# Kernel optimization log

Measured on AMD Instinct MI355X. Metric: run time of the kernel, lower is better.

The kernel has to match this reference:

```python
import jax, jax.numpy as jnp
import numpy as np

B, T, D = 4, 2048, 1024
H = 16
HD = D // H  # 64

def setup_inputs() -> dict:
    key = jax.random.key(0)
    k1, k2, k3, k4, k5 = jax.random.split(key, 5)
    s = 1.0 / np.sqrt(D)
    return {
        "x": jax.random.normal(k1, (B, T, D), dtype=jnp.float32),
        "Wqkv": jax.random.normal(k2, (D, 3 * D), dtype=jnp.float32) * s,
        "bqkv": jnp.zeros((3 * D,), dtype=jnp.float32),
        "Wproj": jax.random.normal(k3, (D, D), dtype=jnp.float32) * s,
        "bproj": jnp.zeros((D,), dtype=jnp.float32),
    }

def reference(x, Wqkv, bqkv, Wproj, bproj):
    Bq, Tq, C = x.shape
    qkv = x @ Wqkv + bqkv                       # [B,T,3D]
    qkv = qkv.reshape(Bq, Tq, 3, H, HD).transpose(2, 0, 3, 1, 4)  # [3,B,H,T,hd]
    q, k, v = qkv[0], qkv[1], qkv[2]
    scale = 1.0 / np.sqrt(HD)
    att = jnp.einsum("bhqd,bhkd->bhqk", q, k) * scale  # [B,H,T,T]
    causal = jnp.tril(jnp.ones((Tq, Tq), dtype=bool))
    att = jnp.where(causal[None, None], att, -jnp.inf)
    att = jax.nn.softmax(att, axis=-1)
    out = jnp.einsum("bhqk,bhkd->bhqd", att, v)        # [B,H,T,hd]
    out = out.transpose(0, 2, 1, 3).reshape(Bq, Tq, C)
    return out @ Wproj + bproj
```

## Files before the change

### kernel.cpp

```cpp
#include <hip/hip_runtime.h>

typedef float f32x4 __attribute__((ext_vector_type(4)));
typedef __bf16 bf16x8 __attribute__((ext_vector_type(8)));
typedef __bf16 bf16x4 __attribute__((ext_vector_type(4)));

#define B_ 4
#define T_ 2048
#define D_ 1024
#define H_ 16
#define HD_ 64

__device__ __forceinline__ void gload_lds16(const void* g, void* l) {
  __builtin_amdgcn_global_load_lds(
      (const __attribute__((address_space(1))) void*)g,
      (__attribute__((address_space(3))) void*)l, 16, 0, 0);
}

__global__ __launch_bounds__(256) void k_cvt_f32_bf16(
    const float* __restrict__ in, __bf16* __restrict__ out, int n4) {
  int i = blockIdx.x * blockDim.x + threadIdx.x;
  int stride = gridDim.x * blockDim.x;
  for (; i < n4; i += stride) {
    float4 v = reinterpret_cast<const float4*>(in)[i];
    bf16x4 o = { (__bf16)v.x, (__bf16)v.y, (__bf16)v.z, (__bf16)v.w };
    reinterpret_cast<bf16x4*>(out)[i] = o;
  }
}

template <typename Tin>
__global__ __launch_bounds__(256) void k_transpose_bf16(
    const Tin* __restrict__ in, __bf16* __restrict__ out,
    int R, int C, long inb, long outb) {
  __shared__ alignas(16) __bf16 lds[64 * 68];
  const int t = threadIdx.x;
  in  += (long)blockIdx.z * inb;
  out += (long)blockIdx.z * outb;
  const int r0 = blockIdx.y * 64, c0 = blockIdx.x * 64;
#pragma unroll
  for (int i = 0; i < 16; ++i) {
    int e = i * 256 + t, row = e >> 6, col = e & 63;
    lds[row * 68 + col] = (__bf16)(float)in[(long)(r0 + row) * C + c0 + col];
  }
  __syncthreads();
#pragma unroll
  for (int i = 0; i < 16; ++i) {
    int e = i * 256 + t, orow = e >> 6, ocol = e & 63;
    out[(long)(c0 + orow) * R + r0 + ocol] = lds[ocol * 68 + orow];
  }
}

template <int EPI>
__global__ __launch_bounds__(256) void k_gemm_bt(
    const __bf16* __restrict__ A, const __bf16* __restrict__ Bt,
    const float* __restrict__ bias, void* __restrict__ Cout,
    __bf16* __restrict__ vout, int M, int N, int K) {
  __shared__ alignas(16) __bf16 As[2][128 * 32];
  __shared__ alignas(16) __bf16 Bs[2][128 * 32];
  const int t = threadIdx.x;
  const int w = t >> 6, l = t & 63;
  const int g = l >> 4, r16 = l & 15;
  const int wr = w >> 1, wc = w & 1;
  const int m0 = blockIdx.y * 128, n0 = blockIdx.x * 128;

  f32x4 acc[4][4];
#pragma unroll
  for (int i = 0; i < 4; ++i)
#pragma unroll
    for (int j = 0; j < 4; ++j) acc[i][j] = (f32x4){0.f, 0.f, 0.f, 0.f};

  const int arow = t >> 2;
  const int acol = ((t & 3) ^ ((t >> 3) & 3)) * 8;
  const char* Ag = (const char*)(A + (long)(m0 + arow) * K + acol);
  const char* Bg = (const char*)(Bt + (long)(n0 + arow) * K + acol);
  const long rowskip = (long)64 * K * 2;
  const int rdsw = (g ^ ((r16 >> 1) & 3)) * 8;

  auto stage = [&](int buf, long koff) {
    char* AsW = (char*)As[buf] + w * 1024;
    char* BsW = (char*)Bs[buf] + w * 1024;
    gload_lds16(Ag + koff, AsW);
    gload_lds16(Ag + koff + rowskip, AsW + 4096);
    gload_lds16(Bg + koff, BsW);
    gload_lds16(Bg + koff + rowskip, BsW + 4096);
  };

  stage(0, 0);
  __syncthreads();

  for (int kt = 0; kt < K; kt += 32) {
    const int cur = (kt >> 5) & 1;
    if (kt + 32 < K) stage(cur ^ 1, (long)(kt + 32) * 2);
    bf16x8 af[4], bfr[4];
#pragma unroll
    for (int mi = 0; mi < 4; ++mi)
      af[mi] = *reinterpret_cast<const bf16x8*>(
          &As[cur][(wr * 64 + mi * 16 + r16) * 32 + rdsw]);
#pragma unroll
    for (int ni = 0; ni < 4; ++ni)
      bfr[ni] = *reinterpret_cast<const bf16x8*>(
          &Bs[cur][(wc * 64 + ni * 16 + r16) * 32 + rdsw]);
    __builtin_amdgcn_s_setprio(1);
#pragma unroll
    for (int mi = 0; mi < 4; ++mi)
#pragma unroll
      for (int ni = 0; ni < 4; ++ni)
        acc[mi][ni] = __builtin_amdgcn_mfma_f32_16x16x32_bf16(af[mi], bfr[ni], acc[mi][ni], 0, 0, 0);
    __builtin_amdgcn_s_setprio(0);
    __syncthreads();
  }

  if (EPI == 0) {
    const int which = n0 >> 10;
    __bf16* qkvb = (__bf16*)Cout;
#pragma unroll
    for (int mi = 0; mi < 4; ++mi) {
#pragma unroll
      for (int ni = 0; ni < 4; ++ni) {
        const int n = n0 + wc * 64 + ni * 16 + r16;
        const float bv = bias[n];
        f32x4 c = acc[mi][ni];
        const int rem = n & 1023, h = rem >> 6, hd = rem & 63;
        const int mbase = m0 + wr * 64 + mi * 16 + g * 4;
        const int b = mbase >> 11, tt0 = mbase & 2047;
        if (which < 2) {
#pragma unroll
          for (int r = 0; r < 4; ++r)
            qkvb[((long)((which * B_ + b) * H_ + h) * T_ + tt0 + r) * HD_ + hd] =
                (__bf16)(c[r] + bv);
        } else {
          bf16x4 pk = { (__bf16)(c[0] + bv), (__bf16)(c[1] + bv),
                        (__bf16)(c[2] + bv), (__bf16)(c[3] + bv) };
          *reinterpret_cast<bf16x4*>(
              &vout[(((long)b * H_ + h) * HD_ + hd) * T_ + tt0]) = pk;
        }
      }
    }
  } else {
    float* O = (float*)Cout;
#pragma unroll
    for (int mi = 0; mi < 4; ++mi) {
#pragma unroll
      for (int ni = 0; ni < 4; ++ni) {
        const int n = n0 + wc * 64 + ni * 16 + r16;
        const float bv = bias[n];
        f32x4 c = acc[mi][ni];
        const int mbase = m0 + wr * 64 + mi * 16 + g * 4;
#pragma unroll
        for (int r = 0; r < 4; ++r) O[(long)(mbase + r) * N + n] = c[r] + bv;
      }
    }
  }
}

__device__ __forceinline__ void soft_side(
    const f32x4 (&s)[4], float& lrun, bool diag, int qrel,
    int g, int r16, bf16x8& pa0, bf16x8& pa1) {
  float p[4][4];
#pragma unroll
  for (int nf = 0; nf < 4; ++nf) {
#pragma unroll
    for (int rr = 0; rr < 4; ++rr) {
      float x = s[nf][rr];
      if (diag) x = (nf * 16 + 4 * g + rr <= qrel + r16) ? x : -1e30f;
      p[nf][rr] = __builtin_amdgcn_exp2f(x);
    }
  }
  const float ps0 = (p[0][0] + p[0][1]) + (p[0][2] + p[0][3]);
  const float ps1 = (p[1][0] + p[1][1]) + (p[1][2] + p[1][3]);
  const float ps2 = (p[2][0] + p[2][1]) + (p[2][2] + p[2][3]);
  const float ps3 = (p[3][0] + p[3][1]) + (p[3][2] + p[3][3]);
  lrun += (ps0 + ps1) + (ps2 + ps3);

  unsigned u[4][2];
#pragma unroll
  for (int nf = 0; nf < 4; ++nf) {
    asm("v_cvt_pk_bf16_f32 %0, %1, %2"
        : "=v"(u[nf][0]) : "v"(p[nf][0]), "v"(p[nf][1]));
    asm("v_cvt_pk_bf16_f32 %0, %1, %2"
        : "=v"(u[nf][1]) : "v"(p[nf][2]), "v"(p[nf][3]));
  }
#pragma unroll
  for (int j = 0; j < 2; ++j) {
    asm("v_permlane32_swap_b32 %0, %1" : "+v"(u[0][j]), "+v"(u[1][j]));
    asm("v_permlane32_swap_b32 %0, %1" : "+v"(u[2][j]), "+v"(u[3][j]));
  }
#pragma unroll
  for (int j = 0; j < 2; ++j) {
    asm("v_permlane16_swap_b32 %0, %1" : "+v"(u[0][j]), "+v"(u[1][j]));
    asm("v_permlane16_swap_b32 %0, %1" : "+v"(u[2][j]), "+v"(u[3][j]));
  }
  union PU { unsigned w[4]; bf16x8 v; };
  PU a0, a1;
  a0.w[0] = u[0][0]; a0.w[1] = u[0][1]; a0.w[2] = u[1][0]; a0.w[3] = u[1][1];
  a1.w[0] = u[2][0]; a1.w[1] = u[2][1]; a1.w[2] = u[3][0]; a1.w[3] = u[3][1];
  pa0 = a0.v;
  pa1 = a1.v;
}

__global__ __launch_bounds__(256) void k_attn(
    const __bf16* __restrict__ q, const __bf16* __restrict__ k,
    const __bf16* __restrict__ vt, __bf16* __restrict__ o) {
  __shared__ alignas(16) __bf16 Ks[2][64 * 64];
  __shared__ alignas(16) __bf16 Vs[2][64 * 64];
  const int t = threadIdx.x, w = t >> 6, l = t & 63;
  const int g = l >> 4, r16 = l & 15;
  const int bh = blockIdx.x;
  const int prmap[16] = {0, 2, 4, 6, 15, 13, 11, 9, 1, 3, 5, 7, 14, 12, 10, 8};
  const int pr = prmap[blockIdx.y];
  const int qtA = 31 - pr, qtB = pr;
  const int qbaseA = qtA * 64 + w * 16;
  const int qbaseB = qtB * 64 + w * 16;
  const float sc = 0.125f * 1.44269504088896341f;

  auto scale8 = [&](bf16x8 v) {
    bf16x8 r;
#pragma unroll
    for (int j = 0; j < 8; ++j) r[j] = (__bf16)((float)v[j] * sc);
    return r;
  };
  const __bf16* qpA = q + ((long)bh * T_ + qbaseA + r16) * HD_ + g * 8;
  const bf16x8 aqA0 = scale8(*reinterpret_cast<const bf16x8*>(qpA));
  const bf16x8 aqA1 = scale8(*reinterpret_cast<const bf16x8*>(qpA + 32));
  const __bf16* qpB = q + ((long)bh * T_ + qbaseB + r16) * HD_ + g * 8;
  const bf16x8 aqB0 = scale8(*reinterpret_cast<const bf16x8*>(qpB));
  const bf16x8 aqB1 = scale8(*reinterpret_cast<const bf16x8*>(qpB + 32));

  f32x4 oA[4], oB[4];
  float lA = 0.f, lB = 0.f;
#pragma unroll
  for (int i = 0; i < 4; ++i) {
    oA[i] = (f32x4){0.f, 0.f, 0.f, 0.f};
    oB[i] = (f32x4){0.f, 0.f, 0.f, 0.f};
  }

  const int srow = t >> 3, sslot = t & 7;
  const int sswz = sslot ^ (srow & 7);
  const char* kg = (const char*)(k + ((long)bh * T_ + srow) * HD_) + sswz * 16;
  const char* vg = (const char*)(vt + ((long)bh * HD_ + srow) * T_) + sswz * 16;

  auto stage = [&](int buf, int kv0) {
    char* Kd = (char*)Ks[buf] + w * 1024;
    char* Vd = (char*)Vs[buf] + w * 1024;
    gload_lds16(kg + (long)kv0 * 128, Kd);
    gload_lds16(kg + (long)kv0 * 128 + 32 * 128, Kd + 4096);
    gload_lds16(vg + (long)kv0 * 2, Vd);
    gload_lds16(vg + (long)kv0 * 2 + 32 * (long)T_ * 2, Vd + 4096);
  };

  stage(0, 0);
  __syncthreads();

  const int ntile = qtA + 1;
  for (int it = 0; it < ntile; ++it) {
    const int cur = it & 1;
    if (it + 1 < ntile) stage(cur ^ 1, (it + 1) * 64);
    const char* Kc = (const char*)Ks[cur];
    const char* Vc = (const char*)Vs[cur];
    const bool doB = (it <= qtB);

    f32x4 sA[4], sB[4];
    __builtin_amdgcn_s_setprio(1);
#pragma unroll
    for (int nf = 0; nf < 4; ++nf) {
      const char* kb = Kc + (nf * 16 + r16) * 128;
      const bf16x8 b0 = *reinterpret_cast<const bf16x8*>(kb + ((g ^ (r16 & 7)) << 4));
      const bf16x8 b1 = *reinterpret_cast<const bf16x8*>(kb + (((4 + g) ^ (r16 & 7)) << 4));
      f32x4 z = (f32x4){0.f, 0.f, 0.f, 0.f};
      z = __builtin_amdgcn_mfma_f32_16x16x32_bf16(b0, aqA0, z, 0, 0, 0);
      z = __builtin_amdgcn_mfma_f32_16x16x32_bf16(b1, aqA1, z, 0, 0, 0);
      sA[nf] = z;
      if (doB) {
        f32x4 zb = (f32x4){0.f, 0.f, 0.f, 0.f};
        zb = __builtin_amdgcn_mfma_f32_16x16x32_bf16(b0, aqB0, zb, 0, 0, 0);
        zb = __builtin_amdgcn_mfma_f32_16x16x32_bf16(b1, aqB1, zb, 0, 0, 0);
        sB[nf] = zb;
      }
    }
    __builtin_amdgcn_s_setprio(0);

    bf16x8 paA0, paA1, paB0, paB1;
    soft_side(sA, lA, it == qtA, qbaseA - it * 64, g, r16, paA0, paA1);
    if (doB)
      soft_side(sB, lB, it == qtB, qbaseB - it * 64, g, r16, paB0, paB1);

    __builtin_amdgcn_s_setprio(1);
#pragma unroll
    for (int nf = 0; nf < 4; ++nf) {
      const char* vb = Vc + (nf * 16 + r16) * 128;
      const bf16x8 v0 = *reinterpret_cast<const bf16x8*>(vb + ((g ^ (r16 & 7)) << 4));
      const bf16x8 v1 = *reinterpret_cast<const bf16x8*>(vb + (((4 + g) ^ (r16 & 7)) << 4));
      oA[nf] = __builtin_amdgcn_mfma_f32_16x16x32_bf16(paA0, v0, oA[nf], 0, 0, 0);
      oA[nf] = __builtin_amdgcn_mfma_f32_16x16x32_bf16(paA1, v1, oA[nf], 0, 0, 0);
      if (doB) {
        oB[nf] = __builtin_amdgcn_mfma_f32_16x16x32_bf16(paB0, v0, oB[nf], 0, 0, 0);
        oB[nf] = __builtin_amdgcn_mfma_f32_16x16x32_bf16(paB1, v1, oB[nf], 0, 0, 0);
      }
    }
    __builtin_amdgcn_s_setprio(0);
    __syncthreads();
  }

  lA += __shfl_xor(lA, 16, 64);
  lA += __shfl_xor(lA, 32, 64);
  lB += __shfl_xor(lB, 16, 64);
  lB += __shfl_xor(lB, 32, 64);
  const float invA = 1.f / lA, invB = 1.f / lB;
  float invAq[4], invBq[4];
#pragma unroll
  for (int rr = 0; rr < 4; ++rr) {
    invAq[rr] = __shfl(invA, 4 * g + rr, 64);
    invBq[rr] = __shfl(invB, 4 * g + rr, 64);
  }
  const int b = bh >> 4, h = bh & 15;
#pragma unroll
  for (int nf = 0; nf < 4; ++nf) {
    const int hd = nf * 16 + r16;
#pragma unroll
    for (int rr = 0; rr < 4; ++rr) {
      const int ttA = qbaseA + g * 4 + rr;
      o[((long)b * T_ + ttA) * D_ + h * HD_ + hd] = (__bf16)(oA[nf][rr] * invAq[rr]);
      const int ttB = qbaseB + g * 4 + rr;
      o[((long)b * T_ + ttB) * D_ + h * HD_ + hd] = (__bf16)(oB[nf][rr] * invBq[rr]);
    }
  }
}

extern "C" void kernel_launch(void* const* d_in, const int* in_sizes, int n_in,
                              void* d_out, int out_size, void* d_ws, size_t ws_size,
                              hipStream_t stream) {
  (void)in_sizes; (void)n_in; (void)out_size; (void)ws_size;
  const float* x     = (const float*)d_in[0];
  const float* Wqkv  = (const float*)d_in[1];
  const float* bqkv  = (const float*)d_in[2];
  const float* Wproj = (const float*)d_in[3];
  const float* bproj = (const float*)d_in[4];
  float* out = (float*)d_out;

  const long MT = (long)B_ * T_;
  __bf16* xb     = (__bf16*)d_ws;
  __bf16* wqkvt  = xb + MT * D_;
  __bf16* wprojt = wqkvt + (long)3 * D_ * D_;
  __bf16* qkvb   = wprojt + (long)D_ * D_;
  __bf16* vtb    = qkvb + (long)2 * B_ * H_ * T_ * HD_;
  __bf16* attno  = vtb + (long)B_ * H_ * HD_ * T_;

  k_cvt_f32_bf16<<<2048, 256, 0, stream>>>(x, xb, (int)(MT * D_ / 4));
  k_transpose_bf16<float><<<dim3(48, 16, 1), 256, 0, stream>>>(Wqkv, wqkvt, D_, 3 * D_, 0, 0);
  k_transpose_bf16<float><<<dim3(16, 16, 1), 256, 0, stream>>>(Wproj, wprojt, D_, D_, 0, 0);
  k_gemm_bt<0><<<dim3(24, 64), 256, 0, stream>>>(xb, wqkvt, bqkv, qkvb, vtb, 8192, 3072, 1024);
  k_attn<<<dim3(64, 16), 256, 0, stream>>>(
      qkvb, qkvb + (long)B_ * H_ * T_ * HD_, vtb, attno);
  k_gemm_bt<1><<<dim3(8, 64), 256, 0, stream>>>(attno, wprojt, bproj, out, nullptr, 8192, 1024, 1024);
}
```

Baseline: 188.8 us.

## Replace paired causal Q-tiles per block with one Q-tile per block

The attention kernel no longer pairs a long and a short causal query tile in one block, where the two tiles shared the K/V staging. Each block now handles a single 64-row query tile, and the grid doubles to 64x32 with the longest tiles launched first. This lowers register pressure and adds parallelism, but each block now loads K/V tiles only for itself. It also relies on descending-size launch order rather than explicit pairing to balance the load.

```diff
diff --git a/kernel.cpp b/kernel.cpp
--- a/kernel.cpp
+++ b/kernel.cpp
@@ -205,11 +205,8 @@
   const int t = threadIdx.x, w = t >> 6, l = t & 63;
   const int g = l >> 4, r16 = l & 15;
   const int bh = blockIdx.x;
-  const int prmap[16] = {0, 2, 4, 6, 15, 13, 11, 9, 1, 3, 5, 7, 14, 12, 10, 8};
-  const int pr = prmap[blockIdx.y];
-  const int qtA = 31 - pr, qtB = pr;
-  const int qbaseA = qtA * 64 + w * 16;
-  const int qbaseB = qtB * 64 + w * 16;
+  const int qt = 31 - blockIdx.y;
+  const int qbase = qt * 64 + w * 16;
   const float sc = 0.125f * 1.44269504088896341f;
 
   auto scale8 = [&](bf16x8 v) {
@@ -218,20 +215,14 @@
     for (int j = 0; j < 8; ++j) r[j] = (__bf16)((float)v[j] * sc);
     return r;
   };
-  const __bf16* qpA = q + ((long)bh * T_ + qbaseA + r16) * HD_ + g * 8;
-  const bf16x8 aqA0 = scale8(*reinterpret_cast<const bf16x8*>(qpA));
-  const bf16x8 aqA1 = scale8(*reinterpret_cast<const bf16x8*>(qpA + 32));
-  const __bf16* qpB = q + ((long)bh * T_ + qbaseB + r16) * HD_ + g * 8;
-  const bf16x8 aqB0 = scale8(*reinterpret_cast<const bf16x8*>(qpB));
-  const bf16x8 aqB1 = scale8(*reinterpret_cast<const bf16x8*>(qpB + 32));
-
-  f32x4 oA[4], oB[4];
-  float lA = 0.f, lB = 0.f;
-#pragma unroll
-  for (int i = 0; i < 4; ++i) {
-    oA[i] = (f32x4){0.f, 0.f, 0.f, 0.f};
-    oB[i] = (f32x4){0.f, 0.f, 0.f, 0.f};
-  }
+  const __bf16* qp = q + ((long)bh * T_ + qbase + r16) * HD_ + g * 8;
+  const bf16x8 aq0 = scale8(*reinterpret_cast<const bf16x8*>(qp));
+  const bf16x8 aq1 = scale8(*reinterpret_cast<const bf16x8*>(qp + 32));
+
+  f32x4 oacc[4];
+  float lrun = 0.f;
+#pragma unroll
+  for (int i = 0; i < 4; ++i) oacc[i] = (f32x4){0.f, 0.f, 0.f, 0.f};
 
   const int srow = t >> 3, sslot = t & 7;
   const int sswz = sslot ^ (srow & 7);
@@ -250,15 +241,14 @@
   stage(0, 0);
   __syncthreads();
 
-  const int ntile = qtA + 1;
+  const int ntile = qt + 1;
   for (int it = 0; it < ntile; ++it) {
     const int cur = it & 1;
     if (it + 1 < ntile) stage(cur ^ 1, (it + 1) * 64);
     const char* Kc = (const char*)Ks[cur];
     const char* Vc = (const char*)Vs[cur];
-    const bool doB = (it <= qtB);
-
-    f32x4 sA[4], sB[4];
+
+    f32x4 s[4];
     __builtin_amdgcn_s_setprio(1);
 #pragma unroll
     for (int nf = 0; nf < 4; ++nf) {
@@ -266,22 +256,14 @@
       const bf16x8 b0 = *reinterpret_cast<const bf16x8*>(kb + ((g ^ (r16 & 7)) << 4));
       const bf16x8 b1 = *reinterpret_cast<const bf16x8*>(kb + (((4 + g) ^ (r16 & 7)) << 4));
       f32x4 z = (f32x4){0.f, 0.f, 0.f, 0.f};
-      z = __builtin_amdgcn_mfma_f32_16x16x32_bf16(b0, aqA0, z, 0, 0, 0);
-      z = __builtin_amdgcn_mfma_f32_16x16x32_bf16(b1, aqA1, z, 0, 0, 0);
-      sA[nf] = z;
-      if (doB) {
-        f32x4 zb = (f32x4){0.f, 0.f, 0.f, 0.f};
-        zb = __builtin_amdgcn_mfma_f32_16x16x32_bf16(b0, aqB0, zb, 0, 0, 0);
-        zb = __builtin_amdgcn_mfma_f32_16x16x32_bf16(b1, aqB1, zb, 0, 0, 0);
-        sB[nf] = zb;
-      }
+      z = __builtin_amdgcn_mfma_f32_16x16x32_bf16(b0, aq0, z, 0, 0, 0);
+      z = __builtin_amdgcn_mfma_f32_16x16x32_bf16(b1, aq1, z, 0, 0, 0);
+      s[nf] = z;
     }
     __builtin_amdgcn_s_setprio(0);
 
-    bf16x8 paA0, paA1, paB0, paB1;
-    soft_side(sA, lA, it == qtA, qbaseA - it * 64, g, r16, paA0, paA1);
-    if (doB)
-      soft_side(sB, lB, it == qtB, qbaseB - it * 64, g, r16, paB0, paB1);
+    bf16x8 pa0, pa1;
+    soft_side(s, lrun, it == qt, qbase - it * 64, g, r16, pa0, pa1);
 
     __builtin_amdgcn_s_setprio(1);
 #pragma unroll
@@ -289,38 +271,27 @@
       const char* vb = Vc + (nf * 16 + r16) * 128;
       const bf16x8 v0 = *reinterpret_cast<const bf16x8*>(vb + ((g ^ (r16 & 7)) << 4));
       const bf16x8 v1 = *reinterpret_cast<const bf16x8*>(vb + (((4 + g) ^ (r16 & 7)) << 4));
-      oA[nf] = __builtin_amdgcn_mfma_f32_16x16x32_bf16(paA0, v0, oA[nf], 0, 0, 0);
-      oA[nf] = __builtin_amdgcn_mfma_f32_16x16x32_bf16(paA1, v1, oA[nf], 0, 0, 0);
-      if (doB) {
-        oB[nf] = __builtin_amdgcn_mfma_f32_16x16x32_bf16(paB0, v0, oB[nf], 0, 0, 0);
-        oB[nf] = __builtin_amdgcn_mfma_f32_16x16x32_bf16(paB1, v1, oB[nf], 0, 0, 0);
-      }
+      oacc[nf] = __builtin_amdgcn_mfma_f32_16x16x32_bf16(pa0, v0, oacc[nf], 0, 0, 0);
+      oacc[nf] = __builtin_amdgcn_mfma_f32_16x16x32_bf16(pa1, v1, oacc[nf], 0, 0, 0);
     }
     __builtin_amdgcn_s_setprio(0);
     __syncthreads();
   }
 
-  lA += __shfl_xor(lA, 16, 64);
-  lA += __shfl_xor(lA, 32, 64);
-  lB += __shfl_xor(lB, 16, 64);
-  lB += __shfl_xor(lB, 32, 64);
-  const float invA = 1.f / lA, invB = 1.f / lB;
-  float invAq[4], invBq[4];
-#pragma unroll
-  for (int rr = 0; rr < 4; ++rr) {
-    invAq[rr] = __shfl(invA, 4 * g + rr, 64);
-    invBq[rr] = __shfl(invB, 4 * g + rr, 64);
-  }
+  lrun += __shfl_xor(lrun, 16, 64);
+  lrun += __shfl_xor(lrun, 32, 64);
+  const float inv = 1.f / lrun;
+  float invq[4];
+#pragma unroll
+  for (int rr = 0; rr < 4; ++rr) invq[rr] = __shfl(inv, 4 * g + rr, 64);
   const int b = bh >> 4, h = bh & 15;
 #pragma unroll
   for (int nf = 0; nf < 4; ++nf) {
     const int hd = nf * 16 + r16;
 #pragma unroll
     for (int rr = 0; rr < 4; ++rr) {
-      const int ttA = qbaseA + g * 4 + rr;
-      o[((long)b * T_ + ttA) * D_ + h * HD_ + hd] = (__bf16)(oA[nf][rr] * invAq[rr]);
-      const int ttB = qbaseB + g * 4 + rr;
-      o[((long)b * T_ + ttB) * D_ + h * HD_ + hd] = (__bf16)(oB[nf][rr] * invBq[rr]);
+      const int tt = qbase + g * 4 + rr;
+      o[((long)b * T_ + tt) * D_ + h * HD_ + hd] = (__bf16)(oacc[nf][rr] * invq[rr]);
     }
   }
 }
@@ -348,7 +319,7 @@
   k_transpose_bf16<float><<<dim3(48, 16, 1), 256, 0, stream>>>(Wqkv, wqkvt, D_, 3 * D_, 0, 0);
   k_transpose_bf16<float><<<dim3(16, 16, 1), 256, 0, stream>>>(Wproj, wprojt, D_, D_, 0, 0);
   k_gemm_bt<0><<<dim3(24, 64), 256, 0, stream>>>(xb, wqkvt, bqkv, qkvb, vtb, 8192, 3072, 1024);
-  k_attn<<<dim3(64, 16), 256, 0, stream>>>(
+  k_attn<<<dim3(64, 32), 256, 0, stream>>>(
       qkvb, qkvb + (long)B_ * H_ * T_ * HD_, vtb, attno);
   k_gemm_bt<1><<<dim3(8, 64), 256, 0, stream>>>(attno, wprojt, bproj, out, nullptr, 8192, 1024, 1024);
 }
```

Measured after the change: 163.8 us, median of 2. 13.3% less time.
